# Kernel optimization log

Measured on AMD Instinct MI355X. Metric: run time of the kernel, lower is better.

## Reference

```python
import jax, jax.numpy as jnp
import numpy as np

BN_EPS = 1e-5

def _gin_mlp(h, wa, ba, wb, bb):
    # 2-layer MLP: Linear -> ReLU -> Linear
    return jax.nn.relu(h @ wa + ba) @ wb + bb

def _gin_conv(x, src, dst, n, wa, ba, wb, bb):
    # GIN aggregation: (1+eps)*x + sum_{j->i} x_j, eps=0 (PyG default)
    agg = jax.ops.segment_sum(x[src], dst, num_segments=n)
    return _gin_mlp(x + agg, wa, ba, wb, bb)

def _batchnorm(h, gamma, beta):
    # track_running_stats=False -> always batch stats, biased variance
    mean = jnp.mean(h, axis=0)
    var = jnp.var(h, axis=0)
    return (h - mean) * jax.lax.rsqrt(var + BN_EPS) * gamma + beta

def setup_inputs() -> dict:
    key = jax.random.key(0)
    ks = jax.random.split(key, 8)
    N, E, F, H, C = 100000, 1600000, 64, 64, 10
    s = 0.05
    return {
        "x": jax.random.normal(ks[0], (N, F), dtype=jnp.float32),
        "edge_index": jax.random.randint(ks[1], (2, E), 0, N, dtype=jnp.int64),
        "w1a": jax.random.normal(ks[2], (F, H), dtype=jnp.float32) * s,
        "b1a": jnp.zeros((H,), jnp.float32),
        "w1b": jax.random.normal(ks[3], (H, H), dtype=jnp.float32) * s,
        "b1b": jnp.zeros((H,), jnp.float32),
        "bn_gamma": jnp.ones((H,), jnp.float32),
        "bn_beta": jnp.zeros((H,), jnp.float32),
        "w2a": jax.random.normal(ks[4], (H, H), dtype=jnp.float32) * s,
        "b2a": jnp.zeros((H,), jnp.float32),
        "w2b": jax.random.normal(ks[5], (H, H), dtype=jnp.float32) * s,
        "b2b": jnp.zeros((H,), jnp.float32),
        "lin_w": jax.random.normal(ks[6], (H, C), dtype=jnp.float32) * s,
        "lin_b": jnp.zeros((C,), jnp.float32),
    }

def reference(x, edge_index, w1a, b1a, w1b, b1b, bn_gamma, bn_beta,
              w2a, b2a, w2b, b2b, lin_w, lin_b):
    n = x.shape[0]
    src, dst = edge_index[0], edge_index[1]
    h1 = _gin_conv(x, src, dst, n, w1a, b1a, w1b, b1b)   # [N, H]
    h1 = _batchnorm(h1, bn_gamma, bn_beta)               # relu1 never applied (faithful)
    h2 = _gin_conv(h1, src, dst, n, w2a, b2a, w2b, b2b)  # [N, H]
    return h2 @ lin_w + lin_b                            # [N, C]
```

## Files before the change

### kernel.cpp

```cpp
#include <hip/hip_runtime.h>
#include <hip/hip_fp16.h>

#define H 64
#define CBS 512
#define CB_BITS 9
#define TILE 8192
#define CAP 9216
#define NSTAT 64

typedef _Float16 f16;
typedef __attribute__((ext_vector_type(8))) _Float16 v8h;
typedef __attribute__((ext_vector_type(4))) float v4f;

__global__ __launch_bounds__(256)
void cvt_init_kernel(const float* __restrict__ x, f16* __restrict__ xh, int total4,
                     int* __restrict__ gcursor, int CB) {
    int i = blockIdx.x * blockDim.x + threadIdx.x;
    if (blockIdx.x == 0) {
        int t = threadIdx.x;
        if (t < CB) gcursor[t * 16] = t * CAP;
    }
    if (i >= total4) return;
    float4 v = ((const float4*)x)[i];
    f16 h0 = (f16)v.x, h1 = (f16)v.y, h2 = (f16)v.z, h3 = (f16)v.w;
    ushort4 pk;
    pk.x = *(unsigned short*)&h0; pk.y = *(unsigned short*)&h1;
    pk.z = *(unsigned short*)&h2; pk.w = *(unsigned short*)&h3;
    ((ushort4*)xh)[i] = pk;
}

__global__ __launch_bounds__(256)
void part_staged_kernel(const int* __restrict__ ei, int* __restrict__ gcursor,
                        int* __restrict__ pairs, int E, int N, int CB) {
    __shared__ int sd[256];
    __shared__ int excl[256];
    __shared__ int gbase[256];
    __shared__ int lcur[256];
    __shared__ int stage[TILE];
    __shared__ unsigned char bin8[TILE];
    int t = threadIdx.x;
    int ntiles = (E + TILE - 1) / TILE;
    for (int tile = blockIdx.x; tile < ntiles; tile += gridDim.x) {
        int base = tile * TILE;
        int cnt = min(TILE, E - base);
        sd[t] = 0;
        __syncthreads();
        for (int i = t; i < cnt; i += 256) {
            int s = ei[base + i];
            int d = ei[E + base + i];
            if ((unsigned)s < (unsigned)N && (unsigned)d < (unsigned)N)
                atomicAdd(&sd[d >> CB_BITS], 1);
        }
        __syncthreads();
        int v = sd[t];
        __syncthreads();
        for (int off = 1; off < 256; off <<= 1) {
            int add = (t >= off) ? sd[t - off] : 0;
            __syncthreads();
            sd[t] += add;
            __syncthreads();
        }
        int ex = sd[t] - v;
        excl[t] = ex;
        lcur[t] = ex;
        if (t < CB && v > 0) gbase[t] = atomicAdd(&gcursor[t * 16], v);
        int tot = sd[255];
        __syncthreads();
        for (int i = t; i < cnt; i += 256) {
            int s = ei[base + i];
            int d = ei[E + base + i];
            if ((unsigned)s < (unsigned)N && (unsigned)d < (unsigned)N) {
                int cb = d >> CB_BITS;
                int pos = atomicAdd(&lcur[cb], 1);
                stage[pos] = s | ((d & (CBS - 1)) << 17);
                bin8[pos] = (unsigned char)cb;
            }
        }
        __syncthreads();
        for (int i = t; i < tot; i += 256) {
            int b8 = bin8[i];
            pairs[gbase[b8] + (i - excl[b8])] = stage[i];
        }
        __syncthreads();
    }
}

__global__ __launch_bounds__(256)
void scan_cb_kernel(const int* __restrict__ gcursor, int* __restrict__ gbb,
                    int* __restrict__ rowptr, int CB, int N) {
    __shared__ int sd[256];
    int t = threadIdx.x;
    int cnt = (t < CB) ? (gcursor[t * 16] - t * CAP) : 0;
    sd[t] = cnt; __syncthreads();
    for (int off = 1; off < 256; off <<= 1) {
        int add = (t >= off) ? sd[t - off] : 0;
        __syncthreads();
        sd[t] += add;
        __syncthreads();
    }
    if (t < CB) gbb[t] = sd[t] - cnt;
    if (t == 0) { gbb[CB] = sd[255]; rowptr[N] = sd[255]; }
}

__global__ __launch_bounds__(256)
void bucket_csr_kernel(const int* __restrict__ pairs, const int* __restrict__ gcursor,
                       const int* __restrict__ gbb,
                       int* __restrict__ ebuf, int* __restrict__ rowptr, int N) {
    __shared__ int hist[CBS];
    __shared__ int cur[CBS];
    __shared__ int sd[256];
    __shared__ int carry_s;
    int b = blockIdx.x;
    int t = threadIdx.x;
    int pb = b * CAP;
    int cnt = gcursor[b * 16] - pb;
    int gb = gbb[b];
    for (int i = t; i < CBS; i += 256) hist[i] = 0;
    if (t == 0) carry_s = 0;
    __syncthreads();
    for (int i = t; i < cnt; i += 256)
        atomicAdd(&hist[(pairs[pb + i] >> 17) & (CBS - 1)], 1);
    __syncthreads();
    for (int start = 0; start < CBS; start += 256) {
        int v = hist[start + t];
        sd[t] = v; __syncthreads();
        for (int off = 1; off < 256; off <<= 1) {
            int add = (t >= off) ? sd[t - off] : 0;
            __syncthreads();
            sd[t] += add;
            __syncthreads();
        }
        int ex = sd[t] - v + carry_s;
        cur[start + t] = ex;
        int node = b * CBS + start + t;
        if (node < N) rowptr[node] = gb + ex;
        __syncthreads();
        if (t == 0) carry_s += sd[255];
        __syncthreads();
    }
    for (int i = t; i < cnt; i += 256) {
        int p = pairs[pb + i];
        int pos = atomicAdd(&cur[(p >> 17) & (CBS - 1)], 1);
        ebuf[gb + pos] = p & 0x1FFFF;
    }
}

__global__ void repack_kernel(const float* __restrict__ W1a, const float* __restrict__ W1b,
                              const float* __restrict__ W2a, const float* __restrict__ W2b,
                              const float* __restrict__ B2b, const float* __restrict__ LW,
                              const float* __restrict__ LB,
                              f16* __restrict__ pk1a, f16* __restrict__ pk1b,
                              f16* __restrict__ pk2a, f16* __restrict__ pkf,
                              float* __restrict__ bf, float* __restrict__ statsR) {
    int t = blockIdx.x * blockDim.x + threadIdx.x;
    if (t < NSTAT * 128) statsR[t] = 0.f;
    if (t < 12288) {
        int m = t >> 12;
        int e = t & 4095;
        int j = e & 7, lane = (e >> 3) & 63, ks = (e >> 9) & 1, nt = e >> 10;
        int row = ks * 32 + ((lane >> 4) & 3) * 8 + j;
        int col = nt * 16 + (lane & 15);
        const float* W = (m == 0) ? W1a : (m == 1) ? W1b : W2a;
        f16* P = (m == 0) ? pk1a : (m == 1) ? pk1b : pk2a;
        P[e] = (f16)W[row * 64 + col];
    } else if (t < 13312) {
        int e = t - 12288;
        int j = e & 7, lane = (e >> 3) & 63, ks = e >> 9;
        int row = ks * 32 + ((lane >> 4) & 3) * 8 + j;
        int col = lane & 15;
        float a = 0.f;
        if (col < 10)
            for (int m = 0; m < H; ++m) a = fmaf(W2b[row * 64 + m], LW[m * 10 + col], a);
        pkf[e] = (f16)a;
    } else if (t < 13322) {
        int c = t - 13312;
        float a = LB[c];
        for (int m = 0; m < H; ++m) a = fmaf(B2b[m], LW[m * 10 + c], a);
        bf[c] = a;
    }
}

__global__ __launch_bounds__(256)
void gather1_kernel(const f16* __restrict__ xh, const int* __restrict__ rowptr,
                    const int* __restrict__ ebuf, f16* __restrict__ bufA, int N) {
    int wid = (int)(((long long)blockIdx.x * blockDim.x + threadIdx.x) >> 6);
    int lane = threadIdx.x & 63;
    if (wid >= N) return;
    int p0 = __builtin_amdgcn_readfirstlane(rowptr[wid]);
    int pe = __builtin_amdgcn_readfirstlane(rowptr[wid + 1]);
    float acc = (float)xh[((long long)wid << 6) + lane];
    int p = p0;
    for (; p + 16 <= pe; p += 16) {
        float v[16];
#pragma unroll
        for (int q = 0; q < 16; ++q)
            v[q] = (float)xh[((long long)ebuf[p + q] << 6) + lane];
        float s0 = ((v[0] + v[1]) + (v[2] + v[3])) + ((v[4] + v[5]) + (v[6] + v[7]));
        float s1 = ((v[8] + v[9]) + (v[10] + v[11])) + ((v[12] + v[13]) + (v[14] + v[15]));
        acc += s0 + s1;
    }
    if (p + 8 <= pe) {
        float v0 = (float)xh[((long long)ebuf[p + 0] << 6) + lane];
        float v1 = (float)xh[((long long)ebuf[p + 1] << 6) + lane];
        float v2 = (float)xh[((long long)ebuf[p + 2] << 6) + lane];
        float v3 = (float)xh[((long long)ebuf[p + 3] << 6) + lane];
        float v4 = (float)xh[((long long)ebuf[p + 4] << 6) + lane];
        float v5 = (float)xh[((long long)ebuf[p + 5] << 6) + lane];
        float v6 = (float)xh[((long long)ebuf[p + 6] << 6) + lane];
        float v7 = (float)xh[((long long)ebuf[p + 7] << 6) + lane];
        acc += ((v0 + v1) + (v2 + v3)) + ((v4 + v5) + (v6 + v7));
        p += 8;
    }
    for (; p < pe; ++p) acc += (float)xh[((long long)ebuf[p] << 6) + lane];
    bufA[((long long)wid << 6) + lane] = (f16)acc;
}

__global__ __launch_bounds__(256)
void gather2_kernel(const f16* __restrict__ h1p, const float* __restrict__ scale,
                    const float* __restrict__ shiftv, const int* __restrict__ rowptr,
                    const int* __restrict__ ebuf, f16* __restrict__ bufC, int N) {
    int wid = (int)(((long long)blockIdx.x * blockDim.x + threadIdx.x) >> 6);
    int lane = threadIdx.x & 63;
    if (wid >= N) return;
    int p0 = __builtin_amdgcn_readfirstlane(rowptr[wid]);
    int pe = __builtin_amdgcn_readfirstlane(rowptr[wid + 1]);
    float acc = (float)h1p[((long long)wid << 6) + lane];
    int p = p0;
    for (; p + 16 <= pe; p += 16) {
        float v[16];
#pragma unroll
        for (int q = 0; q < 16; ++q)
            v[q] = (float)h1p[((long long)ebuf[p + q] << 6) + lane];
        float s0 = ((v[0] + v[1]) + (v[2] + v[3])) + ((v[4] + v[5]) + (v[6] + v[7]));
        float s1 = ((v[8] + v[9]) + (v[10] + v[11])) + ((v[12] + v[13]) + (v[14] + v[15]));
        acc += s0 + s1;
    }
    if (p + 8 <= pe) {
        float v0 = (float)h1p[((long long)ebuf[p + 0] << 6) + lane];
        float v1 = (float)h1p[((long long)ebuf[p + 1] << 6) + lane];
        float v2 = (float)h1p[((long long)ebuf[p + 2] << 6) + lane];
        float v3 = (float)h1p[((long long)ebuf[p + 3] << 6) + lane];
        float v4 = (float)h1p[((long long)ebuf[p + 4] << 6) + lane];
        float v5 = (float)h1p[((long long)ebuf[p + 5] << 6) + lane];
        float v6 = (float)h1p[((long long)ebuf[p + 6] << 6) + lane];
        float v7 = (float)h1p[((long long)ebuf[p + 7] << 6) + lane];
        acc += ((v0 + v1) + (v2 + v3)) + ((v4 + v5) + (v6 + v7));
        p += 8;
    }
    for (; p < pe; ++p) acc += (float)h1p[((long long)ebuf[p] << 6) + lane];
    float degp1 = (float)(pe - p0 + 1);
    bufC[((long long)wid << 6) + lane] = (f16)(acc * scale[lane] + degp1 * shiftv[lane]);
}

__global__ __launch_bounds__(256)
void mlp1_kernel(const f16* __restrict__ bufA, f16* __restrict__ h1p,
                 const f16* __restrict__ pk1a, const f16* __restrict__ pk1b,
                 const float* __restrict__ B1a, const float* __restrict__ B1b,
                 float* __restrict__ statsR, int N) {
    __shared__ f16 Su[4][16 * 72];
    __shared__ f16 Sh[4][16 * 72];
    __shared__ float red[2][4][64];
    int t = threadIdx.x, wv = t >> 6, lane = t & 63;
    int quad = lane >> 4, r16 = lane & 15;
    int node0 = blockIdx.x * 64 + wv * 16;
    int nodeA = node0 + r16;

    v8h a0 = {}, a1 = {};
    if (nodeA < N) {
        a0 = *(const v8h*)(bufA + (size_t)nodeA * 64 + quad * 8);
        a1 = *(const v8h*)(bufA + (size_t)nodeA * 64 + 32 + quad * 8);
    }
#pragma unroll
    for (int nt = 0; nt < 4; ++nt) {
        v8h b0 = *(const v8h*)(pk1a + (((nt * 2 + 0) * 64 + lane) << 3));
        v8h b1 = *(const v8h*)(pk1a + (((nt * 2 + 1) * 64 + lane) << 3));
        v4f c = {0.f, 0.f, 0.f, 0.f};
        c = __builtin_amdgcn_mfma_f32_16x16x32_f16(a0, b0, c, 0, 0, 0);
        c = __builtin_amdgcn_mfma_f32_16x16x32_f16(a1, b1, c, 0, 0, 0);
        float bias = B1a[nt * 16 + r16];
#pragma unroll
        for (int reg = 0; reg < 4; ++reg)
            Su[wv][(quad * 4 + reg) * 72 + nt * 16 + r16] = (f16)fmaxf(c[reg] + bias, 0.f);
    }
    __syncthreads();
    v8h u0 = *(const v8h*)(&Su[wv][r16 * 72 + quad * 8]);
    v8h u1 = *(const v8h*)(&Su[wv][r16 * 72 + 32 + quad * 8]);
#pragma unroll
    for (int nt = 0; nt < 4; ++nt) {
        v8h b0 = *(const v8h*)(pk1b + (((nt * 2 + 0) * 64 + lane) << 3));
        v8h b1 = *(const v8h*)(pk1b + (((nt * 2 + 1) * 64 + lane) << 3));
        v4f c = {0.f, 0.f, 0.f, 0.f};
        c = __builtin_amdgcn_mfma_f32_16x16x32_f16(u0, b0, c, 0, 0, 0);
        c = __builtin_amdgcn_mfma_f32_16x16x32_f16(u1, b1, c, 0, 0, 0);
        float bias = B1b[nt * 16 + r16];
#pragma unroll
        for (int reg = 0; reg < 4; ++reg) {
            int row = quad * 4 + reg;
            bool valid = (node0 + row) < N;
            Sh[wv][row * 72 + nt * 16 + r16] = valid ? (f16)(c[reg] + bias) : (f16)0;
        }
    }
    __syncthreads();
    for (int i = lane; i < 1024; i += 64) {
        int row = i >> 6, col = i & 63;
        int node = node0 + row;
        if (node < N) h1p[(size_t)node * 64 + col] = Sh[wv][row * 72 + col];
    }
    float s = 0.f, s2 = 0.f;
#pragma unroll
    for (int row = 0; row < 16; ++row) {
        float v = (float)Sh[wv][row * 72 + lane];
        s += v;
        s2 = fmaf(v, v, s2);
    }
    red[0][wv][lane] = s;
    red[1][wv][lane] = s2;
    __syncthreads();
    if (wv == 0) {
        float ts  = (red[0][0][lane] + red[0][1][lane]) + (red[0][2][lane] + red[0][3][lane]);
        float ts2 = (red[1][0][lane] + red[1][1][lane]) + (red[1][2][lane] + red[1][3][lane]);
        float* st = statsR + (size_t)(blockIdx.x & (NSTAT - 1)) * 128;
        unsafeAtomicAdd(&st[lane], ts);
        unsafeAtomicAdd(&st[64 + lane], ts2);
    }
}

__global__ void bn_finalize_kernel(const float* __restrict__ statsR,
                                   const float* __restrict__ gamma,
                                   const float* __restrict__ beta,
                                   float* __restrict__ scale, float* __restrict__ shiftv, float n) {
    int f = threadIdx.x;
    if (f >= H) return;
    float s = 0.f, s2 = 0.f;
    for (int r = 0; r < NSTAT; ++r) {
        s  += statsR[r * 128 + f];
        s2 += statsR[r * 128 + 64 + f];
    }
    float mean = s / n;
    float var = s2 / n - mean * mean;
    var = fmaxf(var, 0.f);
    float sc = gamma[f] * rsqrtf(var + 1e-5f);
    scale[f] = sc;
    shiftv[f] = beta[f] - mean * sc;
}

__global__ __launch_bounds__(256)
void mlp2_kernel(const f16* __restrict__ bufC,
                 const f16* __restrict__ pk2a, const f16* __restrict__ pkf,
                 const float* __restrict__ B2a, const float* __restrict__ bf,
                 float* __restrict__ out, int N) {
    __shared__ f16 Su[4][16 * 72];
    int t = threadIdx.x, wv = t >> 6, lane = t & 63;
    int quad = lane >> 4, r16 = lane & 15;
    int node0 = blockIdx.x * 64 + wv * 16;
    int nodeA = node0 + r16;

    v8h a0 = {}, a1 = {};
    if (nodeA < N) {
        a0 = *(const v8h*)(bufC + (size_t)nodeA * 64 + quad * 8);
        a1 = *(const v8h*)(bufC + (size_t)nodeA * 64 + 32 + quad * 8);
    }
#pragma unroll
    for (int nt = 0; nt < 4; ++nt) {
        v8h b0 = *(const v8h*)(pk2a + (((nt * 2 + 0) * 64 + lane) << 3));
        v8h b1 = *(const v8h*)(pk2a + (((nt * 2 + 1) * 64 + lane) << 3));
        v4f c = {0.f, 0.f, 0.f, 0.f};
        c = __builtin_amdgcn_mfma_f32_16x16x32_f16(a0, b0, c, 0, 0, 0);
        c = __builtin_amdgcn_mfma_f32_16x16x32_f16(a1, b1, c, 0, 0, 0);
        float bias = B2a[nt * 16 + r16];
#pragma unroll
        for (int reg = 0; reg < 4; ++reg)
            Su[wv][(quad * 4 + reg) * 72 + nt * 16 + r16] = (f16)fmaxf(c[reg] + bias, 0.f);
    }
    __syncthreads();
    v8h u0 = *(const v8h*)(&Su[wv][r16 * 72 + quad * 8]);
    v8h u1 = *(const v8h*)(&Su[wv][r16 * 72 + 32 + quad * 8]);
    v8h b0 = *(const v8h*)(pkf + ((0 * 64 + lane) << 3));
    v8h b1 = *(const v8h*)(pkf + ((1 * 64 + lane) << 3));
    v4f c = {0.f, 0.f, 0.f, 0.f};
    c = __builtin_amdgcn_mfma_f32_16x16x32_f16(u0, b0, c, 0, 0, 0);
    c = __builtin_amdgcn_mfma_f32_16x16x32_f16(u1, b1, c, 0, 0, 0);
    if (r16 < 10) {
        float bias = bf[r16];
#pragma unroll
        for (int reg = 0; reg < 4; ++reg) {
            int node = node0 + quad * 4 + reg;
            if (node < N) out[(size_t)node * 10 + r16] = c[reg] + bias;
        }
    }
}

extern "C" void kernel_launch(void* const* d_in, const int* in_sizes, int n_in,
                              void* d_out, int out_size, void* d_ws, size_t ws_size,
                              hipStream_t stream) {
    const float* x    = (const float*)d_in[0];
    const int*   ei   = (const int*)d_in[1];
    const float* w1a  = (const float*)d_in[2];
    const float* b1a  = (const float*)d_in[3];
    const float* w1b  = (const float*)d_in[4];
    const float* b1b  = (const float*)d_in[5];
    const float* bng  = (const float*)d_in[6];
    const float* bnb  = (const float*)d_in[7];
    const float* w2a  = (const float*)d_in[8];
    const float* b2a  = (const float*)d_in[9];
    const float* w2b  = (const float*)d_in[10];
    const float* b2b  = (const float*)d_in[11];
    const float* linw = (const float*)d_in[12];
    const float* linb = (const float*)d_in[13];

    int N = in_sizes[0] / H;
    int E = in_sizes[1] / 2;
    int CB = (N + CBS - 1) / CBS;

    size_t NH = (size_t)N * H;
    char*  wsb    = (char*)d_ws;
    f16*   xh     = (f16*)wsb;
    f16*   bufA   = (f16*)(wsb + NH * 2);
    f16*   bufC   = (f16*)(wsb + NH * 4);
    float* stats  = (float*)(wsb + NH * 6);
    float* scale  = stats + 128;
    float* shiftv = stats + 192;
    float* bf     = stats + 256;
    f16*   pk1a   = (f16*)(bf + 16);
    f16*   pk1b   = pk1a + 4096;
    f16*   pk2a   = pk1b + 4096;
    f16*   pkf    = pk2a + 4096;
    int*   gcursor= (int*)(pkf + 1024);
    int*   gbb    = gcursor + 256 * 16;
    int*   rowptr = gbb + 257;
    int*   ebuf   = rowptr + (N + 1);
    int*   pairs  = ebuf + E;
    float* statsR = (float*)pairs;

    int ntiles = (E + TILE - 1) / TILE;

    cvt_init_kernel<<<(int)((NH / 4 + 255) / 256), 256, 0, stream>>>(
        x, xh, (int)(NH / 4), gcursor, CB);
    part_staged_kernel<<<ntiles, 256, 0, stream>>>(ei, gcursor, pairs, E, N, CB);
    scan_cb_kernel<<<1, 256, 0, stream>>>(gcursor, gbb, rowptr, CB, N);
    bucket_csr_kernel<<<CB, 256, 0, stream>>>(pairs, gcursor, gbb, ebuf, rowptr, N);
    repack_kernel<<<(13322 + 255) / 256, 256, 0, stream>>>(
        w1a, w1b, w2a, w2b, b2b, linw, linb, pk1a, pk1b, pk2a, pkf, bf, statsR);

    int gblocks = (int)(((long long)N * 64 + 255) / 256);
    int mblocks = (N + 63) / 64;
    gather1_kernel<<<gblocks, 256, 0, stream>>>(xh, rowptr, ebuf, bufA, N);
    mlp1_kernel<<<mblocks, 256, 0, stream>>>(bufA, bufA, pk1a, pk1b, b1a, b1b, statsR, N);
    bn_finalize_kernel<<<1, 64, 0, stream>>>(statsR, bng, bnb, scale, shiftv, (float)N);

    gather2_kernel<<<gblocks, 256, 0, stream>>>(bufA, scale, shiftv, rowptr, ebuf, bufC, N);
    mlp2_kernel<<<mblocks, 256, 0, stream>>>(bufC, pk2a, pkf, b2a, bf, (float*)d_out, N);
}
```

Before: 265.7 us.

## Gather 8 nodes per wave with 16-byte vector loads per lane

The two CSR gather kernels change from one wavefront per node (each lane loading one f16 feature) to eight nodes per wavefront, with each 8-lane group loading a full 128-byte row as v8h vectors. This cuts the number of memory instructions and makes better use of each load, which targets the load-issue cost of the edge gather. The price is divergence: the loop runs to the largest degree among the eight nodes and masks lanes that finish early. Edge indices are now loaded per lane with a clamped bound.

```diff
diff --git a/kernel.cpp b/kernel.cpp
--- a/kernel.cpp
+++ b/kernel.cpp
@@ -182,74 +182,106 @@
 
 __global__ __launch_bounds__(256)
 void gather1_kernel(const f16* __restrict__ xh, const int* __restrict__ rowptr,
-                    const int* __restrict__ ebuf, f16* __restrict__ bufA, int N) {
+                    const int* __restrict__ ebuf, f16* __restrict__ bufA,
+                    int N, int Em1) {
     int wid = (int)(((long long)blockIdx.x * blockDim.x + threadIdx.x) >> 6);
     int lane = threadIdx.x & 63;
-    if (wid >= N) return;
-    int p0 = __builtin_amdgcn_readfirstlane(rowptr[wid]);
-    int pe = __builtin_amdgcn_readfirstlane(rowptr[wid + 1]);
-    float acc = (float)xh[((long long)wid << 6) + lane];
-    int p = p0;
-    for (; p + 16 <= pe; p += 16) {
-        float v[16];
-#pragma unroll
-        for (int q = 0; q < 16; ++q)
-            v[q] = (float)xh[((long long)ebuf[p + q] << 6) + lane];
-        float s0 = ((v[0] + v[1]) + (v[2] + v[3])) + ((v[4] + v[5]) + (v[6] + v[7]));
-        float s1 = ((v[8] + v[9]) + (v[10] + v[11])) + ((v[12] + v[13]) + (v[14] + v[15]));
-        acc += s0 + s1;
-    }
-    if (p + 8 <= pe) {
-        float v0 = (float)xh[((long long)ebuf[p + 0] << 6) + lane];
-        float v1 = (float)xh[((long long)ebuf[p + 1] << 6) + lane];
-        float v2 = (float)xh[((long long)ebuf[p + 2] << 6) + lane];
-        float v3 = (float)xh[((long long)ebuf[p + 3] << 6) + lane];
-        float v4 = (float)xh[((long long)ebuf[p + 4] << 6) + lane];
-        float v5 = (float)xh[((long long)ebuf[p + 5] << 6) + lane];
-        float v6 = (float)xh[((long long)ebuf[p + 6] << 6) + lane];
-        float v7 = (float)xh[((long long)ebuf[p + 7] << 6) + lane];
-        acc += ((v0 + v1) + (v2 + v3)) + ((v4 + v5) + (v6 + v7));
-        p += 8;
-    }
-    for (; p < pe; ++p) acc += (float)xh[((long long)ebuf[p] << 6) + lane];
-    bufA[((long long)wid << 6) + lane] = (f16)acc;
+    int g = lane >> 3, fl = lane & 7;
+    int node = wid * 8 + g;
+    bool vn = node < N;
+    int p0 = 0, deg = 0;
+    if (vn) {
+        p0 = rowptr[node];
+        deg = rowptr[node + 1] - p0;
+    }
+    int m = deg;
+    m = max(m, __shfl_xor(m, 8));
+    m = max(m, __shfl_xor(m, 16));
+    m = max(m, __shfl_xor(m, 32));
+
+    float a[8];
+    {
+        v8h s = {};
+        if (vn) s = *(const v8h*)(xh + ((size_t)node << 6) + fl * 8);
+#pragma unroll
+        for (int j = 0; j < 8; ++j) a[j] = (float)s[j];
+    }
+    for (int k = 0; k < m; k += 4) {
+        int idx[4];
+#pragma unroll
+        for (int q = 0; q < 4; ++q)
+            idx[q] = ebuf[min(p0 + k + q, Em1)];
+#pragma unroll
+        for (int q = 0; q < 4; ++q) {
+            if (k + q < deg) {
+                v8h v = *(const v8h*)(xh + ((size_t)idx[q] << 6) + fl * 8);
+#pragma unroll
+                for (int j = 0; j < 8; ++j) a[j] += (float)v[j];
+            }
+        }
+    }
+    if (vn) {
+        v8h o;
+#pragma unroll
+        for (int j = 0; j < 8; ++j) o[j] = (f16)a[j];
+        *(v8h*)(bufA + ((size_t)node << 6) + fl * 8) = o;
+    }
 }
 
 __global__ __launch_bounds__(256)
 void gather2_kernel(const f16* __restrict__ h1p, const float* __restrict__ scale,
                     const float* __restrict__ shiftv, const int* __restrict__ rowptr,
-                    const int* __restrict__ ebuf, f16* __restrict__ bufC, int N) {
+                    const int* __restrict__ ebuf, f16* __restrict__ bufC,
+                    int N, int Em1) {
     int wid = (int)(((long long)blockIdx.x * blockDim.x + threadIdx.x) >> 6);
     int lane = threadIdx.x & 63;
-    if (wid >= N) return;
-    int p0 = __builtin_amdgcn_readfirstlane(rowptr[wid]);
-    int pe = __builtin_amdgcn_readfirstlane(rowptr[wid + 1]);
-    float acc = (float)h1p[((long long)wid << 6) + lane];
-    int p = p0;
-    for (; p + 16 <= pe; p += 16) {
-        float v[16];
-#pragma unroll
-        for (int q = 0; q < 16; ++q)
-            v[q] = (float)h1p[((long long)ebuf[p + q] << 6) + lane];
-        float s0 = ((v[0] + v[1]) + (v[2] + v[3])) + ((v[4] + v[5]) + (v[6] + v[7]));
-        float s1 = ((v[8] + v[9]) + (v[10] + v[11])) + ((v[12] + v[13]) + (v[14] + v[15]));
-        acc += s0 + s1;
-    }
-    if (p + 8 <= pe) {
-        float v0 = (float)h1p[((long long)ebuf[p + 0] << 6) + lane];
-        float v1 = (float)h1p[((long long)ebuf[p + 1] << 6) + lane];
-        float v2 = (float)h1p[((long long)ebuf[p + 2] << 6) + lane];
-        float v3 = (float)h1p[((long long)ebuf[p + 3] << 6) + lane];
-        float v4 = (float)h1p[((long long)ebuf[p + 4] << 6) + lane];
-        float v5 = (float)h1p[((long long)ebuf[p + 5] << 6) + lane];
-        float v6 = (float)h1p[((long long)ebuf[p + 6] << 6) + lane];
-        float v7 = (float)h1p[((long long)ebuf[p + 7] << 6) + lane];
-        acc += ((v0 + v1) + (v2 + v3)) + ((v4 + v5) + (v6 + v7));
-        p += 8;
-    }
-    for (; p < pe; ++p) acc += (float)h1p[((long long)ebuf[p] << 6) + lane];
-    float degp1 = (float)(pe - p0 + 1);
-    bufC[((long long)wid << 6) + lane] = (f16)(acc * scale[lane] + degp1 * shiftv[lane]);
+    int g = lane >> 3, fl = lane & 7;
+    int node = wid * 8 + g;
+    bool vn = node < N;
+    int p0 = 0, deg = 0;
+    if (vn) {
+        p0 = rowptr[node];
+        deg = rowptr[node + 1] - p0;
+    }
+    int m = deg;
+    m = max(m, __shfl_xor(m, 8));
+    m = max(m, __shfl_xor(m, 16));
+    m = max(m, __shfl_xor(m, 32));
+
+    float a[8];
+    {
+        v8h s = {};
+        if (vn) s = *(const v8h*)(h1p + ((size_t)node << 6) + fl * 8);
+#pragma unroll
+        for (int j = 0; j < 8; ++j) a[j] = (float)s[j];
+    }
+    for (int k = 0; k < m; k += 4) {
+        int idx[4];
+#pragma unroll
+        for (int q = 0; q < 4; ++q)
+            idx[q] = ebuf[min(p0 + k + q, Em1)];
+#pragma unroll
+        for (int q = 0; q < 4; ++q) {
+            if (k + q < deg) {
+                v8h v = *(const v8h*)(h1p + ((size_t)idx[q] << 6) + fl * 8);
+#pragma unroll
+                for (int j = 0; j < 8; ++j) a[j] += (float)v[j];
+            }
+        }
+    }
+    if (vn) {
+        float4 sc0 = *(const float4*)(scale + fl * 8);
+        float4 sc1 = *(const float4*)(scale + fl * 8 + 4);
+        float4 sh0 = *(const float4*)(shiftv + fl * 8);
+        float4 sh1 = *(const float4*)(shiftv + fl * 8 + 4);
+        float degp1 = (float)(deg + 1);
+        float sc[8] = {sc0.x, sc0.y, sc0.z, sc0.w, sc1.x, sc1.y, sc1.z, sc1.w};
+        float sh[8] = {sh0.x, sh0.y, sh0.z, sh0.w, sh1.x, sh1.y, sh1.z, sh1.w};
+        v8h o;
+#pragma unroll
+        for (int j = 0; j < 8; ++j) o[j] = (f16)(a[j] * sc[j] + degp1 * sh[j]);
+        *(v8h*)(bufC + ((size_t)node << 6) + fl * 8) = o;
+    }
 }
 
 __global__ __launch_bounds__(256)
@@ -442,12 +474,13 @@
     repack_kernel<<<(13322 + 255) / 256, 256, 0, stream>>>(
         w1a, w1b, w2a, w2b, b2b, linw, linb, pk1a, pk1b, pk2a, pkf, bf, statsR);
 
-    int gblocks = (int)(((long long)N * 64 + 255) / 256);
+    int nwaves = (N + 7) / 8;
+    int gblocks = (int)(((long long)nwaves * 64 + 255) / 256);
     int mblocks = (N + 63) / 64;
-    gather1_kernel<<<gblocks, 256, 0, stream>>>(xh, rowptr, ebuf, bufA, N);
+    gather1_kernel<<<gblocks, 256, 0, stream>>>(xh, rowptr, ebuf, bufA, N, E - 1);
     mlp1_kernel<<<mblocks, 256, 0, stream>>>(bufA, bufA, pk1a, pk1b, b1a, b1b, statsR, N);
     bn_finalize_kernel<<<1, 64, 0, stream>>>(statsR, bng, bnb, scale, shiftv, (float)N);
 
-    gather2_kernel<<<gblocks, 256, 0, stream>>>(bufA, scale, shiftv, rowptr, ebuf, bufC, N);
+    gather2_kernel<<<gblocks, 256, 0, stream>>>(bufA, scale, shiftv, rowptr, ebuf, bufC, N, E - 1);
     mlp2_kernel<<<mblocks, 256, 0, stream>>>(bufC, pk2a, pkf, b2a, bf, (float*)d_out, N);
 }
```

New measurement: 247.9 us. 6.7% less time.
